# Optimization experiments

Measured on AMD Instinct MI355X. Metric: run time of the kernel, lower is better.

The kernel has to match this reference:

```python
import jax, jax.numpy as jnp
import numpy as np

N_NODES = 50000
N_EDGES = 800000
IN_CH = 256
HID = 64
OUT_CH = 64
N_LAYERS = 3
ALPHA = 0.1


def _gpr_temp():
    t = ALPHA * (1.0 - ALPHA) ** np.arange(N_LAYERS + 1)
    t[-1] = (1.0 - ALPHA) ** N_LAYERS
    return jnp.asarray(t, dtype=jnp.float32)


def setup_inputs() -> dict:
    key = jax.random.key(0)
    ks = jax.random.split(key, 8)
    x = jax.random.normal(ks[0], (N_NODES, IN_CH), dtype=jnp.float32)
    edge_index = jax.random.randint(ks[1], (2, N_EDGES), 0, N_NODES, dtype=jnp.int64 if jax.config.jax_enable_x64 else jnp.int32).astype(jnp.int32)
    edge_w = jax.random.uniform(ks[2], (N_EDGES,), dtype=jnp.float32)
    # xavier-uniform-ish scales
    W_in = jax.random.normal(ks[3], (IN_CH, HID), dtype=jnp.float32) * (1.0 / np.sqrt(IN_CH))
    b_in = jnp.zeros((HID,), dtype=jnp.float32)
    layer_W = jax.random.normal(ks[4], (N_LAYERS, HID, HID), dtype=jnp.float32) * (1.0 / np.sqrt(HID))
    layer_b = jnp.zeros((N_LAYERS, HID), dtype=jnp.float32)
    W_out = jax.random.normal(ks[5], (HID, OUT_CH), dtype=jnp.float32) * (1.0 / np.sqrt(HID))
    b_out = jnp.zeros((OUT_CH,), dtype=jnp.float32)
    temp = _gpr_temp()
    return {"x": x, "edge_index": edge_index, "edge_w": edge_w, "W_in": W_in,
            "b_in": b_in, "layer_W": layer_W, "layer_b": layer_b,
            "W_out": W_out, "b_out": b_out, "temp": temp}


def reference(x, edge_index, edge_w, W_in, b_in, layer_W, layer_b, W_out, b_out, temp):
    src, dst = edge_index[0], edge_index[1]
    # inlinear
    h = x @ W_in + b_in                      # [N, HID]
    # GPR combination: hidden = sum_k temp[k] * relu(SpMM(linear(h_k)))
    hidden = h * temp[0]
    cur = h
    for i in range(layer_W.shape[0]):
        z = cur @ layer_W[i] + layer_b[i]    # [N, HID]
        m = z[src] * edge_w[:, None]         # gather + edge weight, [E, HID]
        agg = jax.ops.segment_sum(m, dst, num_segments=x.shape[0])  # scatter-sum
        cur = jax.nn.relu(agg)               # dropout is identity in eval mode
        hidden = hidden + cur * temp[i + 1]
    return hidden @ W_out + b_out            # [N, OUT_CH]
```

## Files before the change

kernel.cpp:

```cpp
#include <hip/hip_runtime.h>
#include <hip/hip_bf16.h>

#define NN 50000
#define NE 800000
#define CIN 256
#define HH 64
#define NBINS 196
#define B1 256
#define EPB 3125
#define NGB 782
#define NLB 3125

typedef unsigned long long u64;
typedef __attribute__((ext_vector_type(8))) short short8;
typedef __attribute__((ext_vector_type(4))) float f32x4;

__device__ __forceinline__ float bf2f(ushort u) {
    union { unsigned int i; float f; } v; v.i = ((unsigned int)u) << 16; return v.f;
}
__device__ __forceinline__ ushort f2bf(float f) {
    __hip_bfloat16 b = __float2bfloat16(f);
    return *reinterpret_cast<ushort*>(&b);
}

__global__ __launch_bounds__(256) void k_prep(
    const float* __restrict__ W_in, const float* __restrict__ LW,
    const float* __restrict__ W_out, ushort* __restrict__ Wp)
{
    const int tid = blockIdx.x * 256 + threadIdx.x;
    if (tid < 16384) {
        const int i = tid & 7;
        const int l = (tid >> 3) & 63;
        const int s = (tid >> 9) & 7;
        const int t = tid >> 12;
        const int k = s * 32 + (l >> 4) * 8 + i;
        const int c = t * 16 + (l & 15);
        Wp[tid] = f2bf(W_in[k * HH + c]);
    } else {
        const int q = (tid - 16384) & 4095;
        const int m = (tid - 16384) >> 12;
        const int i = q & 7;
        const int l = (q >> 3) & 63;
        const int s = (q >> 9) & 1;
        const int t = q >> 10;
        const int k = s * 32 + (l >> 4) * 8 + i;
        const int c = t * 16 + (l & 15);
        const float* Wm = (m < 3) ? (LW + m * HH * HH) : W_out;
        Wp[tid] = f2bf(Wm[k * HH + c]);
    }
}

__global__ __launch_bounds__(256) void k_fused(
    const float* __restrict__ x, const ushort* __restrict__ Wp,
    const float* __restrict__ b, const int* __restrict__ dst,
    int* __restrict__ H, ushort* __restrict__ h_bf)
{
    __shared__ int hist[NBINS];
    if (blockIdx.x < B1) {
        for (int t = threadIdx.x; t < NBINS; t += 256) hist[t] = 0;
        __syncthreads();
        const int e0 = blockIdx.x * EPB;
        for (int i = threadIdx.x; i < EPB; i += 256)
            atomicAdd(&hist[dst[e0 + i] >> 8], 1);
        __syncthreads();
        for (int t = threadIdx.x; t < NBINS; t += 256)
            H[t * B1 + blockIdx.x] = hist[t];
        return;
    }
    const int w = threadIdx.x >> 6;
    const int l = threadIdx.x & 63;
    const int R0 = (blockIdx.x - B1) * 64 + w * 16;
    const int arow = R0 + (l & 15);
    const int xrow = (arow < NN) ? arow : (NN - 1);
    const float* xr = x + (size_t)xrow * CIN + (l >> 4) * 8;
    const short8* WpV = (const short8*)Wp;

    f32x4 acc0 = {0,0,0,0}, acc1 = {0,0,0,0}, acc2 = {0,0,0,0}, acc3 = {0,0,0,0};
    #pragma unroll
    for (int s = 0; s < 8; ++s) {
        const float4 xa = *(const float4*)(xr + s * 32);
        const float4 xb = *(const float4*)(xr + s * 32 + 4);
        short8 af;
        af[0] = (short)f2bf(xa.x); af[1] = (short)f2bf(xa.y);
        af[2] = (short)f2bf(xa.z); af[3] = (short)f2bf(xa.w);
        af[4] = (short)f2bf(xb.x); af[5] = (short)f2bf(xb.y);
        af[6] = (short)f2bf(xb.z); af[7] = (short)f2bf(xb.w);
        acc0 = __builtin_amdgcn_mfma_f32_16x16x32_bf16(af, WpV[(0*8+s)*64 + l], acc0, 0, 0, 0);
        acc1 = __builtin_amdgcn_mfma_f32_16x16x32_bf16(af, WpV[(1*8+s)*64 + l], acc1, 0, 0, 0);
        acc2 = __builtin_amdgcn_mfma_f32_16x16x32_bf16(af, WpV[(2*8+s)*64 + l], acc2, 0, 0, 0);
        acc3 = __builtin_amdgcn_mfma_f32_16x16x32_bf16(af, WpV[(3*8+s)*64 + l], acc3, 0, 0, 0);
    }
    const int colb = l & 15;
    const int rbase = R0 + (l >> 4) * 4;
    #pragma unroll
    for (int t = 0; t < 4; ++t) {
        const f32x4 a = (t == 0) ? acc0 : (t == 1) ? acc1 : (t == 2) ? acc2 : acc3;
        const float bb = b[t * 16 + colb];
        #pragma unroll
        for (int r = 0; r < 4; ++r) {
            const int row = rbase + r;
            if (row < NN)
                h_bf[(size_t)row * HH + t * 16 + colb] = f2bf(a[r] + bb);
        }
    }
}

__global__ __launch_bounds__(256) void k_scanS(
    const int* __restrict__ H, int* __restrict__ Sx, int* __restrict__ bcnt)
{
    __shared__ int s[256];
    const int t = threadIdx.x;
    int rowsum = 0;
    if (t < NBINS) {
        const int4* row = (const int4*)(H + t * B1);
        #pragma unroll 8
        for (int c = 0; c < B1 / 4; ++c) {
            const int4 v = row[c];
            rowsum += v.x + v.y + v.z + v.w;
        }
    }
    s[t] = (t < NBINS) ? rowsum : 0;
    __syncthreads();
    #pragma unroll
    for (int off = 1; off < 256; off <<= 1) {
        const int add = (t >= off) ? s[t - off] : 0;
        __syncthreads();
        s[t] += add;
        __syncthreads();
    }
    if (t < NBINS) {
        Sx[t] = s[t] - rowsum;
        bcnt[t] = rowsum;
    }
}

__global__ __launch_bounds__(256) void k_scanW(
    int* __restrict__ H, const int* __restrict__ Sx)
{
    __shared__ int s[256];
    const int b = blockIdx.x;
    const int t = threadIdx.x;
    const int v = H[b * B1 + t];
    s[t] = v;
    __syncthreads();
    #pragma unroll
    for (int off = 1; off < 256; off <<= 1) {
        const int add = (t >= off) ? s[t - off] : 0;
        __syncthreads();
        s[t] += add;
        __syncthreads();
    }
    H[b * B1 + t] = s[t] - v + Sx[b];
}

__global__ __launch_bounds__(256) void k_scatterA(
    const int* __restrict__ src, const int* __restrict__ dst,
    const float* __restrict__ ew, const int* __restrict__ H,
    int2* __restrict__ tmp_e, ushort* __restrict__ tmp_low)
{
    __shared__ int cur[NBINS];
    for (int t = threadIdx.x; t < NBINS; t += 256)
        cur[t] = H[t * B1 + blockIdx.x];
    __syncthreads();
    const int e0 = blockIdx.x * EPB;
    for (int i = threadIdx.x; i < EPB; i += 256) {
        const int e = e0 + i;
        const int d = dst[e];
        const int pos = atomicAdd(&cur[d >> 8], 1);
        tmp_e[pos] = make_int2(src[e], __float_as_int(ew[e]));
        tmp_low[pos] = (ushort)(d & 255);
    }
}

__global__ __launch_bounds__(512) void k_sortB(
    const int2* __restrict__ tmp_e, const ushort* __restrict__ tmp_low,
    const int* __restrict__ Sx, const int* __restrict__ bcnt,
    int2* __restrict__ epack, int* __restrict__ rowptr, int* __restrict__ cnt)
{
    __shared__ int hist[256], s[256], curs[256];
    const int b = blockIdx.x;
    const int base = Sx[b];
    const int cntE = bcnt[b];
    const int t = threadIdx.x;
    if (t < 256) hist[t] = 0;
    __syncthreads();
    for (int i = t; i < cntE; i += 512)
        atomicAdd(&hist[tmp_low[base + i]], 1);
    __syncthreads();
    if (t < 256) s[t] = hist[t];
    __syncthreads();
    #pragma unroll
    for (int off = 1; off < 256; off <<= 1) {
        const int add = (t < 256 && t >= off) ? s[t - off] : 0;
        __syncthreads();
        if (t < 256) s[t] += add;
        __syncthreads();
    }
    if (t < 256) {
        const int excl = s[t] - hist[t];
        curs[t] = excl;
        const int d = b * 256 + t;
        if (d < NN) { rowptr[d] = base + excl; cnt[d] = hist[t]; }
    }
    __syncthreads();
    for (int i = t; i < cntE; i += 512) {
        const int2 e = tmp_e[base + i];
        const int low = (int)tmp_low[base + i];
        const int pos = base + atomicAdd(&curs[low], 1);
        epack[pos] = e;
    }
}

template<bool FINAL>
__global__ __launch_bounds__(256) void k_layer(
    const ushort* __restrict__ cur_in, ushort* __restrict__ cur_out,
    const int2* __restrict__ epack, const int* __restrict__ rowptr,
    const int* __restrict__ cnt,
    const ushort* __restrict__ WpL, const float* __restrict__ bvec,
    const float* __restrict__ temp,
    const ushort* __restrict__ hbf, const ushort* __restrict__ c1,
    const ushort* __restrict__ WpO, const float* __restrict__ bout,
    float* __restrict__ outp)
{
    __shared__ int2  es[4][64];
    __shared__ ushort ts[16][72];
    __shared__ float swv[16];
    const int w = threadIdx.x >> 6;
    const int j = threadIdx.x & 63;
    const int nb = blockIdx.x * 16;

    int rsA[4], rcA[4];
    #pragma unroll
    for (int q = 0; q < 4; ++q) {
        rsA[q] = rowptr[nb + w * 4 + q];
        rcA[q] = cnt[nb + w * 4 + q];
    }
    int2 pf = epack[min(rsA[0] + ((j < rcA[0]) ? j : 0), NE - 1)];

    #pragma unroll
    for (int q = 0; q < 4; ++q) {
        const int rs = rsA[q];
        const int rc = rcA[q];
        es[w][j] = pf;
        if (q < 3)
            pf = epack[min(rsA[q+1] + ((j < rcA[q+1]) ? j : 0), NE - 1)];

        float acc = 0.0f;
        float sw  = 0.0f;
        const int m0 = min(rc, 64);
        for (int g = 0; g < m0; g += 8) {
            float vv[8], ww[8];
            #pragma unroll
            for (int u = 0; u < 8; ++u) {
                const int idx = g + u;
                const int sel = (idx < m0) ? idx : 0;
                const int2 p = es[w][sel];
                ww[u] = (idx < m0) ? __int_as_float(p.y) : 0.0f;
                vv[u] = bf2f(cur_in[(size_t)p.x * HH + j]);
            }
            #pragma unroll
            for (int u = 0; u < 8; ++u) { acc = fmaf(ww[u], vv[u], acc); sw += ww[u]; }
        }
        for (int base = 64; base < rc; base += 64) {
            const int m = min(rc - base, 64);
            if (j < m) es[w][j] = epack[rs + base + j];
            for (int g = 0; g < m; g += 8) {
                float vv[8], ww[8];
                #pragma unroll
                for (int u = 0; u < 8; ++u) {
                    const int idx = g + u;
                    const int sel = (idx < m) ? idx : 0;
                    const int2 p = es[w][sel];
                    ww[u] = (idx < m) ? __int_as_float(p.y) : 0.0f;
                    vv[u] = bf2f(cur_in[(size_t)p.x * HH + j]);
                }
                #pragma unroll
                for (int u = 0; u < 8; ++u) { acc = fmaf(ww[u], vv[u], acc); sw += ww[u]; }
            }
        }
        ts[w * 4 + q][j] = f2bf(acc);
        if (j == 0) swv[w * 4 + q] = sw;
    }
    __syncthreads();

    const int lr = j & 15;
    const int lg = j >> 4;
    const short8 a0 = *(const short8*)&ts[lr][lg * 8];
    const short8 a1 = *(const short8*)&ts[lr][32 + lg * 8];
    if (FINAL) __syncthreads();

    const short8* WpV = (const short8*)WpL;
    f32x4 zac = {0,0,0,0};
    zac = __builtin_amdgcn_mfma_f32_16x16x32_bf16(a0, WpV[(w*2+0)*64 + j], zac, 0, 0, 0);
    zac = __builtin_amdgcn_mfma_f32_16x16x32_bf16(a1, WpV[(w*2+1)*64 + j], zac, 0, 0, 0);

    const float bb = bvec[w * 16 + lr];
    float t0v = 0, t1v = 0, t2v = 0, t3v = 0;
    if (FINAL) { t0v = temp[0]; t1v = temp[1]; t2v = temp[2]; t3v = temp[3]; }
    #pragma unroll
    for (int r = 0; r < 4; ++r) {
        const int row = lg * 4 + r;
        const int n   = nb + row;
        const float z = zac[r] + swv[row] * bb;
        const float rv = fmaxf(z, 0.0f);
        const size_t o = (size_t)n * HH + w * 16 + lr;
        if (!FINAL) {
            cur_out[o] = f2bf(rv);
        } else {
            const float hid = t0v * bf2f(hbf[o]) + t1v * bf2f(c1[o])
                            + t2v * bf2f(cur_in[o]) + t3v * rv;
            ts[row][w * 16 + lr] = f2bf(hid);
        }
    }
    if (FINAL) {
        __syncthreads();
        const short8 b0 = *(const short8*)&ts[lr][lg * 8];
        const short8 b1 = *(const short8*)&ts[lr][32 + lg * 8];
        const short8* WoV = (const short8*)WpO;
        f32x4 oz = {0,0,0,0};
        oz = __builtin_amdgcn_mfma_f32_16x16x32_bf16(b0, WoV[(w*2+0)*64 + j], oz, 0, 0, 0);
        oz = __builtin_amdgcn_mfma_f32_16x16x32_bf16(b1, WoV[(w*2+1)*64 + j], oz, 0, 0, 0);
        const float bo = bout[w * 16 + lr];
        #pragma unroll
        for (int r = 0; r < 4; ++r) {
            const int row = lg * 4 + r;
            outp[(size_t)(nb + row) * HH + w * 16 + lr] = oz[r] + bo;
        }
    }
}

extern "C" void kernel_launch(void* const* d_in, const int* in_sizes, int n_in,
                              void* d_out, int out_size, void* d_ws, size_t ws_size,
                              hipStream_t stream)
{
    const float* x     = (const float*)d_in[0];
    const int*   ei    = (const int*)d_in[1];
    const float* ew    = (const float*)d_in[2];
    const float* W_in  = (const float*)d_in[3];
    const float* b_in  = (const float*)d_in[4];
    const float* LW    = (const float*)d_in[5];
    const float* Lb    = (const float*)d_in[6];
    const float* W_out = (const float*)d_in[7];
    const float* b_out = (const float*)d_in[8];
    const float* temp  = (const float*)d_in[9];
    const int* src = ei;
    const int* dst = ei + NE;

    char* p = (char*)d_ws;
    ushort* h_bf    = (ushort*)p;  p += (size_t)NN * HH * 2;
    ushort* curA    = (ushort*)p;  p += (size_t)NN * HH * 2;
    ushort* curB    = (ushort*)p;  p += (size_t)NN * HH * 2;
    int2*   epack   = (int2*)p;    p += (size_t)NE * 8;
    int2*   tmp_e   = (int2*)p;    p += (size_t)NE * 8;
    ushort* tmp_low = (ushort*)p;  p += (size_t)NE * 2;
    int*    H       = (int*)p;     p += (size_t)NBINS * B1 * 4;
    int*    Sx      = (int*)p;     p += (NBINS + 1) * 4;
    int*    bcnt    = (int*)p;     p += NBINS * 4;
    int*    rowptr  = (int*)p;     p += (size_t)NN * 4;
    int*    cnt     = (int*)p;     p += (size_t)NN * 4;
    ushort* Wp      = (ushort*)p;  p += 32768 * 2;
    float*  out     = (float*)d_out;

    const ushort* WpIn  = Wp;
    const ushort* WpL0  = Wp + 16384;
    const ushort* WpL1  = Wp + 16384 + 4096;
    const ushort* WpL2  = Wp + 16384 + 2 * 4096;
    const ushort* WpOut = Wp + 16384 + 3 * 4096;

    k_prep<<<128, 256, 0, stream>>>(W_in, LW, W_out, Wp);
    k_fused<<<B1 + NGB, 256, 0, stream>>>(x, WpIn, b_in, dst, H, h_bf);
    k_scanS<<<1, 256, 0, stream>>>(H, Sx, bcnt);
    k_scanW<<<NBINS, 256, 0, stream>>>(H, Sx);
    k_scatterA<<<B1, 256, 0, stream>>>(src, dst, ew, H, tmp_e, tmp_low);
    k_sortB<<<NBINS, 512, 0, stream>>>(tmp_e, tmp_low, Sx, bcnt, epack, rowptr, cnt);

    k_layer<false><<<NLB, 256, 0, stream>>>(h_bf, curA, epack, rowptr, cnt,
                                            WpL0, Lb + 0 * HH, temp,
                                            nullptr, nullptr, nullptr, nullptr, nullptr);
    k_layer<false><<<NLB, 256, 0, stream>>>(curA, curB, epack, rowptr, cnt,
                                            WpL1, Lb + 1 * HH, temp,
                                            nullptr, nullptr, nullptr, nullptr, nullptr);
    k_layer<true><<<NLB, 256, 0, stream>>>(curB, nullptr, epack, rowptr, cnt,
                                           WpL2, Lb + 2 * HH, temp,
                                           h_bf, curA, WpOut, b_out, out);
}
```

Before: 135.2 us.

## Merge scan kernels and vectorize SpMM gather with 4-channel lanes

The two-kernel bin scan becomes a single kernel. Each block recomputes its prefix base by summing all preceding histogram entries, which removes one launch and one serial dependency at the cost of redundant reads. The SpMM gather in the layer kernel now has each lane load 4 bf16 channels (8 bytes) for one of 4 edges per step instead of 2 bytes per lane. Partial sums are then combined with cross-lane shuffles, giving wider memory transactions and more edges in flight per wavefront in exchange for extra shuffle reductions.

```diff
diff --git a/kernel.cpp b/kernel.cpp
--- a/kernel.cpp
+++ b/kernel.cpp
@@ -105,41 +105,23 @@
     }
 }
 
-__global__ __launch_bounds__(256) void k_scanS(
-    const int* __restrict__ H, int* __restrict__ Sx, int* __restrict__ bcnt)
-{
-    __shared__ int s[256];
-    const int t = threadIdx.x;
-    int rowsum = 0;
-    if (t < NBINS) {
-        const int4* row = (const int4*)(H + t * B1);
-        #pragma unroll 8
-        for (int c = 0; c < B1 / 4; ++c) {
-            const int4 v = row[c];
-            rowsum += v.x + v.y + v.z + v.w;
-        }
-    }
-    s[t] = (t < NBINS) ? rowsum : 0;
-    __syncthreads();
-    #pragma unroll
-    for (int off = 1; off < 256; off <<= 1) {
-        const int add = (t >= off) ? s[t - off] : 0;
-        __syncthreads();
-        s[t] += add;
-        __syncthreads();
-    }
-    if (t < NBINS) {
-        Sx[t] = s[t] - rowsum;
-        bcnt[t] = rowsum;
-    }
-}
-
-__global__ __launch_bounds__(256) void k_scanW(
-    int* __restrict__ H, const int* __restrict__ Sx)
+__global__ __launch_bounds__(256) void k_scan(
+    int* __restrict__ H, int* __restrict__ Sx, int* __restrict__ bcnt)
 {
     __shared__ int s[256];
     const int b = blockIdx.x;
     const int t = threadIdx.x;
+    int partial = 0;
+    for (int idx = t; idx < b * B1; idx += 256) partial += H[idx];
+    s[t] = partial;
+    __syncthreads();
+    #pragma unroll
+    for (int off = 128; off > 0; off >>= 1) {
+        if (t < off) s[t] += s[t + off];
+        __syncthreads();
+    }
+    const int base = s[0];
+    __syncthreads();
     const int v = H[b * B1 + t];
     s[t] = v;
     __syncthreads();
@@ -150,7 +132,8 @@
         s[t] += add;
         __syncthreads();
     }
-    H[b * B1 + t] = s[t] - v + Sx[b];
+    H[b * B1 + t] = s[t] - v + base;
+    if (t == 255) { Sx[b] = base; bcnt[b] = s[255]; }
 }
 
 __global__ __launch_bounds__(256) void k_scatterA(
@@ -228,6 +211,8 @@
     const int w = threadIdx.x >> 6;
     const int j = threadIdx.x & 63;
     const int nb = blockIdx.x * 16;
+    const int cg  = j >> 4;
+    const int ch4 = j & 15;
 
     int rsA[4], rcA[4];
     #pragma unroll
@@ -245,41 +230,59 @@
         if (q < 3)
             pf = epack[min(rsA[q+1] + ((j < rcA[q+1]) ? j : 0), NE - 1)];
 
-        float acc = 0.0f;
-        float sw  = 0.0f;
+        float4 acc = {0.0f, 0.0f, 0.0f, 0.0f};
+        float  sw  = 0.0f;
         const int m0 = min(rc, 64);
-        for (int g = 0; g < m0; g += 8) {
-            float vv[8], ww[8];
+        for (int g = 0; g < m0; g += 16) {
             #pragma unroll
-            for (int u = 0; u < 8; ++u) {
-                const int idx = g + u;
+            for (int u = 0; u < 4; ++u) {
+                const int idx = g + u * 4 + cg;
                 const int sel = (idx < m0) ? idx : 0;
                 const int2 p = es[w][sel];
-                ww[u] = (idx < m0) ? __int_as_float(p.y) : 0.0f;
-                vv[u] = bf2f(cur_in[(size_t)p.x * HH + j]);
+                const float wgt = (idx < m0) ? __int_as_float(p.y) : 0.0f;
+                const uint2 v = *(const uint2*)(cur_in + (size_t)p.x * HH + ch4 * 4);
+                acc.x = fmaf(wgt, bf2f((ushort)(v.x & 0xffff)), acc.x);
+                acc.y = fmaf(wgt, bf2f((ushort)(v.x >> 16)),    acc.y);
+                acc.z = fmaf(wgt, bf2f((ushort)(v.y & 0xffff)), acc.z);
+                acc.w = fmaf(wgt, bf2f((ushort)(v.y >> 16)),    acc.w);
+                sw += wgt;
             }
-            #pragma unroll
-            for (int u = 0; u < 8; ++u) { acc = fmaf(ww[u], vv[u], acc); sw += ww[u]; }
         }
         for (int base = 64; base < rc; base += 64) {
             const int m = min(rc - base, 64);
             if (j < m) es[w][j] = epack[rs + base + j];
-            for (int g = 0; g < m; g += 8) {
-                float vv[8], ww[8];
+            for (int g = 0; g < m; g += 16) {
                 #pragma unroll
-                for (int u = 0; u < 8; ++u) {
-                    const int idx = g + u;
+                for (int u = 0; u < 4; ++u) {
+                    const int idx = g + u * 4 + cg;
                     const int sel = (idx < m) ? idx : 0;
                     const int2 p = es[w][sel];
-                    ww[u] = (idx < m) ? __int_as_float(p.y) : 0.0f;
-                    vv[u] = bf2f(cur_in[(size_t)p.x * HH + j]);
+                    const float wgt = (idx < m) ? __int_as_float(p.y) : 0.0f;
+                    const uint2 v = *(const uint2*)(cur_in + (size_t)p.x * HH + ch4 * 4);
+                    acc.x = fmaf(wgt, bf2f((ushort)(v.x & 0xffff)), acc.x);
+                    acc.y = fmaf(wgt, bf2f((ushort)(v.x >> 16)),    acc.y);
+                    acc.z = fmaf(wgt, bf2f((ushort)(v.y & 0xffff)), acc.z);
+                    acc.w = fmaf(wgt, bf2f((ushort)(v.y >> 16)),    acc.w);
+                    sw += wgt;
                 }
-                #pragma unroll
-                for (int u = 0; u < 8; ++u) { acc = fmaf(ww[u], vv[u], acc); sw += ww[u]; }
             }
         }
-        ts[w * 4 + q][j] = f2bf(acc);
-        if (j == 0) swv[w * 4 + q] = sw;
+        #pragma unroll
+        for (int off = 16; off < 64; off <<= 1) {
+            acc.x += __shfl_xor(acc.x, off);
+            acc.y += __shfl_xor(acc.y, off);
+            acc.z += __shfl_xor(acc.z, off);
+            acc.w += __shfl_xor(acc.w, off);
+            sw    += __shfl_xor(sw, off);
+        }
+        if (j < 16) {
+            const int node = w * 4 + q;
+            uint2 o;
+            o.x = (uint)f2bf(acc.x) | ((uint)f2bf(acc.y) << 16);
+            o.y = (uint)f2bf(acc.z) | ((uint)f2bf(acc.w) << 16);
+            *(uint2*)&ts[node][ch4 * 4] = o;
+            if (j == 0) swv[node] = sw;
+        }
     }
     __syncthreads();
 
@@ -369,8 +372,7 @@
 
     k_prep<<<128, 256, 0, stream>>>(W_in, LW, W_out, Wp);
     k_fused<<<B1 + NGB, 256, 0, stream>>>(x, WpIn, b_in, dst, H, h_bf);
-    k_scanS<<<1, 256, 0, stream>>>(H, Sx, bcnt);
-    k_scanW<<<NBINS, 256, 0, stream>>>(H, Sx);
+    k_scan<<<NBINS, 256, 0, stream>>>(H, Sx, bcnt);
     k_scatterA<<<B1, 256, 0, stream>>>(src, dst, ew, H, tmp_e, tmp_low);
     k_sortB<<<NBINS, 512, 0, stream>>>(tmp_e, tmp_low, Sx, bcnt, epack, rowptr, cnt);
 
```

After: 134.7 us. Within noise of the previous version (-0.3%).
